# Kernel optimization log

Measured on AMD Instinct MI355X. Metric: run time of the kernel, lower is better.

## Reference

```python
import jax, jax.numpy as jnp
import numpy as np

MAXV = 8  # convex quad clipped by 4 half-planes has <= 8 vertices


def decode(enc, anchors):
    """ResidualCoder.decode_torch for 7-dof lidar boxes (x,y,z,dx,dy,dz,r)."""
    xa, ya, za, dxa, dya, dza, ra = [anchors[..., i] for i in range(7)]
    xt, yt, zt, dxt, dyt, dzt, rt = [enc[..., i] for i in range(7)]
    diag = jnp.sqrt(dxa * dxa + dya * dya)
    xg = xt * diag + xa
    yg = yt * diag + ya
    zg = zt * dza + za
    dxg = jnp.exp(dxt) * dxa
    dyg = jnp.exp(dyt) * dya
    dzg = jnp.exp(dzt) * dza
    rg = rt + ra
    return jnp.stack([xg, yg, zg, dxg, dyg, dzg, rg], axis=-1)


def bev_corners(boxes):
    # boxes (...,7) -> CCW BEV corners (...,4,2) using x,y,dx,dy,heading
    x, y, dx, dy, r = boxes[..., 0], boxes[..., 1], boxes[..., 3], boxes[..., 4], boxes[..., 6]
    cx = jnp.stack([dx, -dx, -dx, dx], -1) * 0.5
    cy = jnp.stack([dy, dy, -dy, -dy], -1) * 0.5
    c, s = jnp.cos(r)[..., None], jnp.sin(r)[..., None]
    px = cx * c - cy * s + x[..., None]
    py = cx * s + cy * c + y[..., None]
    return jnp.stack([px, py], -1)


def _clip(poly, n, A, B):
    """Sutherland-Hodgman clip of polygon (poly[:n]) by half-plane left of A->B."""
    idx = jnp.arange(MAXV)
    e = B - A
    s = e[0] * (poly[:, 1] - A[1]) - e[1] * (poly[:, 0] - A[0])  # signed side
    prev = (idx - 1) % jnp.maximum(n, 1)
    s_prev = s[prev]
    p_prev = poly[prev]
    active = idx < n
    cin = s >= 0
    pin = s_prev >= 0
    den = s_prev - s
    t = s_prev / jnp.where(den == 0, 1.0, den)
    inter = p_prev + t[:, None] * (poly - p_prev)
    f_int = active & (cin != pin)   # edge crosses boundary -> emit intersection
    f_cur = active & cin            # current vertex inside -> emit it
    cand = jnp.stack([inter, poly], 1).reshape(2 * MAXV, 2)
    flags = jnp.stack([f_int, f_cur], 1).reshape(2 * MAXV)
    pos = jnp.cumsum(flags) - 1
    new_n = pos[-1] + 1
    pos = jnp.where(flags, pos, MAXV)  # invalid -> dump slot
    out = jnp.zeros((MAXV + 1, 2), poly.dtype).at[pos].set(cand)[:MAXV]
    return out, new_n.astype(jnp.int32)


def _pair_iou_bev(c1, c2, a1, a2):
    # c1,c2: (4,2) CCW corners of the two rotated BEV boxes; a1,a2: scalar areas
    poly = jnp.zeros((MAXV, 2), c1.dtype).at[:4].set(c1)
    n = jnp.asarray(4, jnp.int32)
    for e in range(4):
        poly, n = _clip(poly, n, c2[e], c2[(e + 1) % 4])
    idx = jnp.arange(MAXV)
    nxt = (idx + 1) % jnp.maximum(n, 1)
    x, y = poly[:, 0], poly[:, 1]
    contrib = jnp.where(idx < n, x * y[nxt] - x[nxt] * y, 0.0)
    inter = 0.5 * jnp.abs(contrib.sum())
    return inter / jnp.clip(a1 + a2 - inter, 1e-6, None)


def rotated_iou_bev_diag(boxes1, boxes2):
    """Diagonal (elementwise) rotated BEV IoU for flattened (M,7) lidar boxes."""
    c1 = bev_corners(boxes1)
    c2 = bev_corners(boxes2)
    a1 = boxes1[..., 3] * boxes1[..., 4]
    a2 = boxes2[..., 3] * boxes2[..., 4]
    return jax.vmap(_pair_iou_bev)(c1, c2, a1, a2)


def setup_inputs() -> dict:
    key = jax.random.key(0)
    ks = jax.random.split(key, 8)
    B, N = 4, 262144
    iou_preds = jax.random.normal(ks[0], (B, N), jnp.float32)
    one_hot_targets = jax.random.randint(ks[1], (B, N), 0, 2, jnp.int32)
    weights = jax.random.uniform(ks[2], (B, N), jnp.float32)
    # realistic anchors: xy in [-50,50], z ~ -1, dims in [1.5,4.5], heading in [0,pi)
    xy = jax.random.uniform(ks[3], (N, 2), jnp.float32, -50.0, 50.0)
    z = jnp.full((N, 1), -1.0, jnp.float32)
    dims = jax.random.uniform(ks[4], (N, 3), jnp.float32, 1.5, 4.5)
    ang = jax.random.uniform(ks[5], (N, 1), jnp.float32, 0.0, np.pi)
    anchors = jnp.concatenate([xy, z, dims, ang], axis=-1)
    box_preds = 0.1 * jax.random.normal(ks[6], (B, N, 7), jnp.float32)
    reg_targets = 0.1 * jax.random.normal(ks[7], (B, N, 7), jnp.float32)
    return {"iou_preds": iou_preds, "one_hot_targets": one_hot_targets,
            "weights": weights, "anchors": anchors,
            "box_preds": box_preds, "reg_targets": reg_targets}


def reference(iou_preds, one_hot_targets, weights, anchors, box_preds, reg_targets):
    B, N = iou_preds.shape
    dec_pred = decode(box_preds, anchors[None, :, :])   # (B,N,7)
    dec_tgt = decode(reg_targets, anchors[None, :, :])  # (B,N,7)
    iou = rotated_iou_bev_diag(dec_pred.reshape(B * N, 7),
                               dec_tgt.reshape(B * N, 7)).reshape(B, N)
    # label is computed with no grad, only at positive anchors; zero elsewhere
    target = jax.lax.stop_gradient(jnp.where(one_hot_targets > 0, iou, 0.0))
    # faithful to the original quirk: BCE-with-logits applied to sigmoid(iou_preds)
    z = jax.nn.sigmoid(iou_preds)
    p_t = jnp.logaddexp(0.0, z) - z * target  # log(1+e^z) - t*z
    return p_t * weights
```

## Files before the change

kernel.cpp:

```cpp
#include <hip/hip_runtime.h>
#include <math.h>

#define BLK 256
#define MAXV 8


__device__ __forceinline__ void clip_first(float* __restrict__ PX, float* __restrict__ PY,
                                           int tid,
                                           const float qx[4], const float qy[4],
                                           int& n, float& lastx, float& lasty,
                                           float Ax, float Ay, float Bx, float By)
{
    float ex = Bx - Ax, ey = By - Ay;
    float s0 = ex * (qy[0] - Ay) - ey * (qx[0] - Ax);
    float s1 = ex * (qy[1] - Ay) - ey * (qx[1] - Ax);
    float s2 = ex * (qy[2] - Ay) - ey * (qx[2] - Ax);
    float s3 = ex * (qy[3] - Ay) - ey * (qx[3] - Ax);
    float vs[4] = {s0, s1, s2, s3};

    float ppx = qx[3], ppy = qy[3], ps = s3;
    int m = 0;
    float lx = ppx, ly = ppy;
#pragma unroll
    for (int i = 0; i < 4; ++i) {
        float cx = qx[i], cy = qy[i], cs = vs[i];
        bool cin = (cs >= 0.0f), pin = (ps >= 0.0f);
        if (cin != pin) {
            float den = ps - cs;
            den = (den == 0.0f) ? 1.0f : den;
            float t = __fdividef(ps, den);
            float ix = fmaf(t, cx - ppx, ppx);
            float iy = fmaf(t, cy - ppy, ppy);
            if (m < MAXV) { PX[m * BLK + tid] = ix; PY[m * BLK + tid] = iy; }
            lx = ix; ly = iy; ++m;
        }
        if (cin) {
            if (m < MAXV) { PX[m * BLK + tid] = cx; PY[m * BLK + tid] = cy; }
            lx = cx; ly = cy; ++m;
        }
        ppx = cx; ppy = cy; ps = cs;
    }
    n = (m < MAXV) ? m : MAXV;
    lastx = lx; lasty = ly;
}

template<int NIN>
__device__ __forceinline__ void clip_mid(float* __restrict__ PX, float* __restrict__ PY,
                                         int tid, int& n, float& lastx, float& lasty,
                                         float Ax, float Ay, float Bx, float By)
{
    float ex = Bx - Ax, ey = By - Ay;
    float vx[NIN], vy[NIN], vs[NIN];
#pragma unroll
    for (int i = 0; i < NIN; ++i) {
        vx[i] = PX[i * BLK + tid];
        vy[i] = PY[i * BLK + tid];
        vs[i] = ex * (vy[i] - Ay) - ey * (vx[i] - Ax);
    }
    float ppx = lastx, ppy = lasty;
    float ps = ex * (ppy - Ay) - ey * (ppx - Ax);
    int m = 0;
    float lx = lastx, ly = lasty;
#pragma unroll
    for (int i = 0; i < NIN; ++i) {
        if (i < n) {
            float cx = vx[i], cy = vy[i], cs = vs[i];
            bool cin = (cs >= 0.0f), pin = (ps >= 0.0f);
            if (cin != pin) {
                float den = ps - cs;
                den = (den == 0.0f) ? 1.0f : den;
                float t = __fdividef(ps, den);
                float ix = fmaf(t, cx - ppx, ppx);
                float iy = fmaf(t, cy - ppy, ppy);
                if (m < MAXV) { PX[m * BLK + tid] = ix; PY[m * BLK + tid] = iy; }
                lx = ix; ly = iy; ++m;
            }
            if (cin) {
                if (m < MAXV) { PX[m * BLK + tid] = cx; PY[m * BLK + tid] = cy; }
                lx = cx; ly = cy; ++m;
            }
            ppx = cx; ppy = cy; ps = cs;
        }
    }
    n = (m < MAXV) ? m : MAXV;
    lastx = lx; lasty = ly;
}

template<int NIN>
__device__ __forceinline__ float clip_area(const float* __restrict__ PX,
                                           const float* __restrict__ PY,
                                           int tid, int n, float lastx, float lasty,
                                           float Ax, float Ay, float Bx, float By)
{
    float ex = Bx - Ax, ey = By - Ay;
    float ppx = lastx, ppy = lasty;
    float ps = ex * (ppy - Ay) - ey * (ppx - Ax);
    int m = 0;
    float fx = 0.0f, fy = 0.0f, lx = 0.0f, ly = 0.0f, area2 = 0.0f;
#pragma unroll
    for (int i = 0; i < NIN; ++i) {
        if (i < n) {
            float cx = PX[i * BLK + tid], cy = PY[i * BLK + tid];
            float cs = ex * (cy - Ay) - ey * (cx - Ax);
            bool cin = (cs >= 0.0f), pin = (ps >= 0.0f);
            if (cin != pin) {
                float den = ps - cs;
                den = (den == 0.0f) ? 1.0f : den;
                float t = __fdividef(ps, den);
                float ix = fmaf(t, cx - ppx, ppx);
                float iy = fmaf(t, cy - ppy, ppy);
                if (m == 0) { fx = ix; fy = iy; }
                else        { area2 += lx * iy - ix * ly; }
                lx = ix; ly = iy; ++m;
            }
            if (cin) {
                if (m == 0) { fx = cx; fy = cy; }
                else        { area2 += lx * cy - cx * ly; }
                lx = cx; ly = cy; ++m;
            }
            ppx = cx; ppy = cy; ps = cs;
        }
    }
    if (m > 0) area2 += lx * fy - fx * ly;
    return 0.5f * fabsf(area2);
}

__global__ __launch_bounds__(BLK)
void iou_pred_loss_kernel(const float* __restrict__ iou_preds,
                          const int*   __restrict__ one_hot,
                          const float* __restrict__ weights,
                          const float* __restrict__ anchors,
                          const float* __restrict__ box_preds,
                          const float* __restrict__ reg_targets,
                          float* __restrict__ out,
                          int N, int total)
{
    __shared__ float sPX[MAXV][BLK];
    __shared__ float sPY[MAXV][BLK];

    int tid = threadIdx.x;
    int gid = blockIdx.x * BLK + tid;
    if (gid >= total) return;

    int n_idx = gid % N;

    const float* an = anchors + (size_t)n_idx * 7;
    float xa = an[0], ya = an[1], dxa = an[3], dya = an[4], ra = an[6];
    float diag = sqrtf(dxa * dxa + dya * dya);

    const float* bp = box_preds + (size_t)gid * 7;
    float x1  = fmaf(bp[0], diag, xa);
    float y1  = fmaf(bp[1], diag, ya);
    float dx1 = __expf(bp[3]) * dxa;
    float dy1 = __expf(bp[4]) * dya;
    float r1  = bp[6] + ra;

    const float* rt = reg_targets + (size_t)gid * 7;
    float x2  = fmaf(rt[0], diag, xa);
    float y2  = fmaf(rt[1], diag, ya);
    float dx2 = __expf(rt[3]) * dxa;
    float dy2 = __expf(rt[4]) * dya;
    float r2  = rt[6] + ra;

    float a1 = dx1 * dy1;
    float a2 = dx2 * dy2;

    float c1 = __cosf(r1), s1 = __sinf(r1);
    float hx1 = 0.5f * dx1, hy1 = 0.5f * dy1;
    float q1x[4], q1y[4];
    q1x[0] =  hx1 * c1 - hy1 * s1 + x1;  q1y[0] =  hx1 * s1 + hy1 * c1 + y1;
    q1x[1] = -hx1 * c1 - hy1 * s1 + x1;  q1y[1] = -hx1 * s1 + hy1 * c1 + y1;
    q1x[2] = -hx1 * c1 + hy1 * s1 + x1;  q1y[2] = -hx1 * s1 - hy1 * c1 + y1;
    q1x[3] =  hx1 * c1 + hy1 * s1 + x1;  q1y[3] =  hx1 * s1 - hy1 * c1 + y1;

    float c2 = __cosf(r2), s2 = __sinf(r2);
    float hx2 = 0.5f * dx2, hy2 = 0.5f * dy2;
    float q2x[4], q2y[4];
    q2x[0] =  hx2 * c2 - hy2 * s2 + x2;  q2y[0] =  hx2 * s2 + hy2 * c2 + y2;
    q2x[1] = -hx2 * c2 - hy2 * s2 + x2;  q2y[1] = -hx2 * s2 + hy2 * c2 + y2;
    q2x[2] = -hx2 * c2 + hy2 * s2 + x2;  q2y[2] = -hx2 * s2 - hy2 * c2 + y2;
    q2x[3] =  hx2 * c2 + hy2 * s2 + x2;  q2y[3] =  hx2 * s2 - hy2 * c2 + y2;

    float* PX = &sPX[0][0];
    float* PY = &sPY[0][0];
    int   n;
    float lastx, lasty;
    clip_first(PX, PY, tid, q1x, q1y, n, lastx, lasty,
               q2x[0], q2y[0], q2x[1], q2y[1]);
    clip_mid<6>(PX, PY, tid, n, lastx, lasty,
                q2x[1], q2y[1], q2x[2], q2y[2]);
    clip_mid<7>(PX, PY, tid, n, lastx, lasty,
                q2x[2], q2y[2], q2x[3], q2y[3]);
    float inter = clip_area<8>(PX, PY, tid, n, lastx, lasty,
                               q2x[3], q2y[3], q2x[0], q2y[0]);

    float uni = a1 + a2 - inter;
    uni = fmaxf(uni, 1e-6f);
    float iou = __fdividef(inter, uni);

    float target = (one_hot[gid] > 0) ? iou : 0.0f;
    float ip = iou_preds[gid];
    float z  = __fdividef(1.0f, 1.0f + __expf(-ip));
    float pt = __logf(1.0f + __expf(z)) - z * target;
    out[gid] = pt * weights[gid];
}

extern "C" void kernel_launch(void* const* d_in, const int* in_sizes, int n_in,
                              void* d_out, int out_size, void* d_ws, size_t ws_size,
                              hipStream_t stream) {
    const float* iou_preds   = (const float*)d_in[0];
    const int*   one_hot     = (const int*)  d_in[1];
    const float* weights     = (const float*)d_in[2];
    const float* anchors     = (const float*)d_in[3];
    const float* box_preds   = (const float*)d_in[4];
    const float* reg_targets = (const float*)d_in[5];
    float* out = (float*)d_out;

    int total = in_sizes[0];
    int N     = in_sizes[3] / 7;

    int blocks = (total + BLK - 1) / BLK;
    iou_pred_loss_kernel<<<blocks, BLK, 0, stream>>>(
        iou_preds, one_hot, weights, anchors, box_preds, reg_targets,
        out, N, total);
}
```

Before: 123.7 us.

## Clip in box-2 local frame with axis-aligned half-planes and branchless writes

Transforms box 1 into box 2's local coordinate frame, so the four clipping half-planes become axis-aligned tests (K - y, x + K, etc.) rather than general edge cross-products. The clip loops become branchless by writing to a spare shared-memory slot when a vertex is not emitted, and polygon vertices are stored as float2. The grid becomes 2D (anchor by batch), which removes the integer modulo. This cuts arithmetic and wavefront divergence, at the cost of always doing the divisions and stores and of small rounding differences from the changed frame.

```diff
diff --git a/kernel.cpp b/kernel.cpp
--- a/kernel.cpp
+++ b/kernel.cpp
@@ -2,126 +2,121 @@
 #include <math.h>
 
 #define BLK 256
-#define MAXV 8
-
-
-__device__ __forceinline__ void clip_first(float* __restrict__ PX, float* __restrict__ PY,
-                                           int tid,
-                                           const float qx[4], const float qy[4],
-                                           int& n, float& lastx, float& lasty,
-                                           float Ax, float Ay, float Bx, float By)
-{
-    float ex = Bx - Ax, ey = By - Ay;
-    float s0 = ex * (qy[0] - Ay) - ey * (qx[0] - Ax);
-    float s1 = ex * (qy[1] - Ay) - ey * (qx[1] - Ax);
-    float s2 = ex * (qy[2] - Ay) - ey * (qx[2] - Ax);
-    float s3 = ex * (qy[3] - Ay) - ey * (qx[3] - Ax);
-    float vs[4] = {s0, s1, s2, s3};
-
-    float ppx = qx[3], ppy = qy[3], ps = s3;
-    int m = 0;
-    float lx = ppx, ly = ppy;
+#define SPARE 8
+
+
+template<int MODE>
+__device__ __forceinline__ float sfun(float x, float y, float K) {
+    if (MODE == 0) return K - y;
+    if (MODE == 1) return x + K;
+    if (MODE == 2) return y + K;
+    return K - x;
+}
+
+template<int MODE>
+__device__ __forceinline__ int clip_first(float2* __restrict__ P, int tid,
+                                          const float qx[4], const float qy[4],
+                                          float K)
+{
+    float ppx = qx[3], ppy = qy[3];
+    float ps  = sfun<MODE>(ppx, ppy, K);
+    bool  pin = ps >= 0.0f;
+    int   m   = 0;
 #pragma unroll
     for (int i = 0; i < 4; ++i) {
-        float cx = qx[i], cy = qy[i], cs = vs[i];
-        bool cin = (cs >= 0.0f), pin = (ps >= 0.0f);
-        if (cin != pin) {
-            float den = ps - cs;
-            den = (den == 0.0f) ? 1.0f : den;
-            float t = __fdividef(ps, den);
-            float ix = fmaf(t, cx - ppx, ppx);
-            float iy = fmaf(t, cy - ppy, ppy);
-            if (m < MAXV) { PX[m * BLK + tid] = ix; PY[m * BLK + tid] = iy; }
-            lx = ix; ly = iy; ++m;
-        }
-        if (cin) {
-            if (m < MAXV) { PX[m * BLK + tid] = cx; PY[m * BLK + tid] = cy; }
-            lx = cx; ly = cy; ++m;
-        }
-        ppx = cx; ppy = cy; ps = cs;
-    }
-    n = (m < MAXV) ? m : MAXV;
-    lastx = lx; lasty = ly;
-}
-
-template<int NIN>
-__device__ __forceinline__ void clip_mid(float* __restrict__ PX, float* __restrict__ PY,
-                                         int tid, int& n, float& lastx, float& lasty,
-                                         float Ax, float Ay, float Bx, float By)
-{
-    float ex = Bx - Ax, ey = By - Ay;
+        float cx = qx[i], cy = qy[i];
+        float cs = sfun<MODE>(cx, cy, K);
+        bool  cin = cs >= 0.0f;
+        bool  fi  = (cin != pin);
+        float t  = __fdividef(ps, ps - cs);
+        float ix = fmaf(t, cx - ppx, ppx);
+        float iy = fmaf(t, cy - ppy, ppy);
+        int si = fi ? m : SPARE;
+        P[si * BLK + tid] = make_float2(ix, iy);
+        m += fi;
+        int sc = cin ? m : SPARE;
+        P[sc * BLK + tid] = make_float2(cx, cy);
+        m += cin;
+        ppx = cx; ppy = cy; ps = cs; pin = cin;
+    }
+    return m;
+}
+
+template<int MODE, int NIN>
+__device__ __forceinline__ int clip_mid(float2* __restrict__ P, int tid,
+                                        int n, float K)
+{
     float vx[NIN], vy[NIN], vs[NIN];
 #pragma unroll
     for (int i = 0; i < NIN; ++i) {
-        vx[i] = PX[i * BLK + tid];
-        vy[i] = PY[i * BLK + tid];
-        vs[i] = ex * (vy[i] - Ay) - ey * (vx[i] - Ax);
-    }
-    float ppx = lastx, ppy = lasty;
-    float ps = ex * (ppy - Ay) - ey * (ppx - Ax);
-    int m = 0;
-    float lx = lastx, ly = lasty;
+        float2 v = P[i * BLK + tid];
+        vx[i] = v.x; vy[i] = v.y;
+        vs[i] = sfun<MODE>(v.x, v.y, K);
+    }
+    int pslot = n - 1; pslot = pslot < 0 ? 0 : pslot;
+    float2 pv = P[pslot * BLK + tid];
+    float ppx = pv.x, ppy = pv.y;
+    float ps  = sfun<MODE>(ppx, ppy, K);
+    bool  pin = ps >= 0.0f;
+    int   m   = 0;
 #pragma unroll
     for (int i = 0; i < NIN; ++i) {
-        if (i < n) {
-            float cx = vx[i], cy = vy[i], cs = vs[i];
-            bool cin = (cs >= 0.0f), pin = (ps >= 0.0f);
-            if (cin != pin) {
-                float den = ps - cs;
-                den = (den == 0.0f) ? 1.0f : den;
-                float t = __fdividef(ps, den);
-                float ix = fmaf(t, cx - ppx, ppx);
-                float iy = fmaf(t, cy - ppy, ppy);
-                if (m < MAXV) { PX[m * BLK + tid] = ix; PY[m * BLK + tid] = iy; }
-                lx = ix; ly = iy; ++m;
-            }
-            if (cin) {
-                if (m < MAXV) { PX[m * BLK + tid] = cx; PY[m * BLK + tid] = cy; }
-                lx = cx; ly = cy; ++m;
-            }
-            ppx = cx; ppy = cy; ps = cs;
-        }
-    }
-    n = (m < MAXV) ? m : MAXV;
-    lastx = lx; lasty = ly;
-}
-
-template<int NIN>
-__device__ __forceinline__ float clip_area(const float* __restrict__ PX,
-                                           const float* __restrict__ PY,
-                                           int tid, int n, float lastx, float lasty,
-                                           float Ax, float Ay, float Bx, float By)
-{
-    float ex = Bx - Ax, ey = By - Ay;
-    float ppx = lastx, ppy = lasty;
-    float ps = ex * (ppy - Ay) - ey * (ppx - Ax);
-    int m = 0;
+        bool  act = i < n;
+        float cx = vx[i], cy = vy[i], cs = vs[i];
+        bool  cin = cs >= 0.0f;
+        bool  fi  = act && (cin != pin);
+        bool  fc  = act && cin;
+        float t  = __fdividef(ps, ps - cs);
+        float ix = fmaf(t, cx - ppx, ppx);
+        float iy = fmaf(t, cy - ppy, ppy);
+        int si = fi ? m : SPARE;
+        P[si * BLK + tid] = make_float2(ix, iy);
+        m += fi;
+        int sc = fc ? m : SPARE;
+        P[sc * BLK + tid] = make_float2(cx, cy);
+        m += fc;
+        ppx = cx; ppy = cy; ps = cs; pin = cin;
+    }
+    return m;
+}
+
+template<int MODE, int NIN>
+__device__ __forceinline__ float clip_area(const float2* __restrict__ P, int tid,
+                                           int n, float K)
+{
+    int pslot = n - 1; pslot = pslot < 0 ? 0 : pslot;
+    float2 pv = P[pslot * BLK + tid];
+    float ppx = pv.x, ppy = pv.y;
+    float ps  = sfun<MODE>(ppx, ppy, K);
+    bool  pin = ps >= 0.0f;
+    bool  seen = false;
     float fx = 0.0f, fy = 0.0f, lx = 0.0f, ly = 0.0f, area2 = 0.0f;
 #pragma unroll
     for (int i = 0; i < NIN; ++i) {
-        if (i < n) {
-            float cx = PX[i * BLK + tid], cy = PY[i * BLK + tid];
-            float cs = ex * (cy - Ay) - ey * (cx - Ax);
-            bool cin = (cs >= 0.0f), pin = (ps >= 0.0f);
-            if (cin != pin) {
-                float den = ps - cs;
-                den = (den == 0.0f) ? 1.0f : den;
-                float t = __fdividef(ps, den);
-                float ix = fmaf(t, cx - ppx, ppx);
-                float iy = fmaf(t, cy - ppy, ppy);
-                if (m == 0) { fx = ix; fy = iy; }
-                else        { area2 += lx * iy - ix * ly; }
-                lx = ix; ly = iy; ++m;
-            }
-            if (cin) {
-                if (m == 0) { fx = cx; fy = cy; }
-                else        { area2 += lx * cy - cx * ly; }
-                lx = cx; ly = cy; ++m;
-            }
-            ppx = cx; ppy = cy; ps = cs;
-        }
-    }
-    if (m > 0) area2 += lx * fy - fx * ly;
+        float2 v = P[i * BLK + tid];
+        float cx = v.x, cy = v.y;
+        float cs = sfun<MODE>(cx, cy, K);
+        bool  act = i < n;
+        bool  cin = cs >= 0.0f;
+        bool  fi  = act && (cin != pin);
+        bool  fc  = act && cin;
+        float t  = __fdividef(ps, ps - cs);
+        float ix = fmaf(t, cx - ppx, ppx);
+        float iy = fmaf(t, cy - ppy, ppy);
+        float c1 = fmaf(lx, iy, -(ix * ly));
+        area2 += (fi && seen) ? c1 : 0.0f;
+        fx = (fi && !seen) ? ix : fx;  fy = (fi && !seen) ? iy : fy;
+        lx = fi ? ix : lx;             ly = fi ? iy : ly;
+        seen = seen || fi;
+        float c2 = fmaf(lx, cy, -(cx * ly));
+        area2 += (fc && seen) ? c2 : 0.0f;
+        fx = (fc && !seen) ? cx : fx;  fy = (fc && !seen) ? cy : fy;
+        lx = fc ? cx : lx;             ly = fc ? cy : ly;
+        seen = seen || fc;
+        ppx = cx; ppy = cy; ps = cs; pin = cin;
+    }
+    float wrap = fmaf(lx, fy, -(fx * ly));
+    area2 += seen ? wrap : 0.0f;
     return 0.5f * fabsf(area2);
 }
 
@@ -133,20 +128,18 @@
                           const float* __restrict__ box_preds,
                           const float* __restrict__ reg_targets,
                           float* __restrict__ out,
-                          int N, int total)
-{
-    __shared__ float sPX[MAXV][BLK];
-    __shared__ float sPY[MAXV][BLK];
-
-    int tid = threadIdx.x;
-    int gid = blockIdx.x * BLK + tid;
-    if (gid >= total) return;
-
-    int n_idx = gid % N;
+                          int N)
+{
+    __shared__ float2 sP[(SPARE + 1) * BLK];
+
+    int tid   = threadIdx.x;
+    int n_idx = blockIdx.x * BLK + tid;
+    if (n_idx >= N) return;
+    int gid = blockIdx.y * N + n_idx;
 
     const float* an = anchors + (size_t)n_idx * 7;
     float xa = an[0], ya = an[1], dxa = an[3], dya = an[4], ra = an[6];
-    float diag = sqrtf(dxa * dxa + dya * dya);
+    float diag = sqrtf(fmaf(dxa, dxa, dya * dya));
 
     const float* bp = box_preds + (size_t)gid * 7;
     float x1  = fmaf(bp[0], diag, xa);
@@ -165,34 +158,29 @@
     float a1 = dx1 * dy1;
     float a2 = dx2 * dy2;
 
-    float c1 = __cosf(r1), s1 = __sinf(r1);
-    float hx1 = 0.5f * dx1, hy1 = 0.5f * dy1;
-    float q1x[4], q1y[4];
-    q1x[0] =  hx1 * c1 - hy1 * s1 + x1;  q1y[0] =  hx1 * s1 + hy1 * c1 + y1;
-    q1x[1] = -hx1 * c1 - hy1 * s1 + x1;  q1y[1] = -hx1 * s1 + hy1 * c1 + y1;
-    q1x[2] = -hx1 * c1 + hy1 * s1 + x1;  q1y[2] = -hx1 * s1 - hy1 * c1 + y1;
-    q1x[3] =  hx1 * c1 + hy1 * s1 + x1;  q1y[3] =  hx1 * s1 - hy1 * c1 + y1;
-
-    float c2 = __cosf(r2), s2 = __sinf(r2);
-    float hx2 = 0.5f * dx2, hy2 = 0.5f * dy2;
-    float q2x[4], q2y[4];
-    q2x[0] =  hx2 * c2 - hy2 * s2 + x2;  q2y[0] =  hx2 * s2 + hy2 * c2 + y2;
-    q2x[1] = -hx2 * c2 - hy2 * s2 + x2;  q2y[1] = -hx2 * s2 + hy2 * c2 + y2;
-    q2x[2] = -hx2 * c2 + hy2 * s2 + x2;  q2y[2] = -hx2 * s2 - hy2 * c2 + y2;
-    q2x[3] =  hx2 * c2 + hy2 * s2 + x2;  q2y[3] =  hx2 * s2 - hy2 * c2 + y2;
-
-    float* PX = &sPX[0][0];
-    float* PY = &sPY[0][0];
-    int   n;
-    float lastx, lasty;
-    clip_first(PX, PY, tid, q1x, q1y, n, lastx, lasty,
-               q2x[0], q2y[0], q2x[1], q2y[1]);
-    clip_mid<6>(PX, PY, tid, n, lastx, lasty,
-                q2x[1], q2y[1], q2x[2], q2y[2]);
-    clip_mid<7>(PX, PY, tid, n, lastx, lasty,
-                q2x[2], q2y[2], q2x[3], q2y[3]);
-    float inter = clip_area<8>(PX, PY, tid, n, lastx, lasty,
-                               q2x[3], q2y[3], q2x[0], q2y[0]);
+    float c2v = __cosf(r2), s2v = __sinf(r2);
+    float dr  = r1 - r2;
+    float cd  = __cosf(dr), sd = __sinf(dr);
+    float ddx = x1 - x2, ddy = y1 - y2;
+    float tx  = fmaf(c2v, ddx,  s2v * ddy);
+    float ty  = fmaf(-s2v, ddx, c2v * ddy);
+    float h1x = 0.5f * dx1, h1y = 0.5f * dy1;
+    float h2x = 0.5f * dx2, h2y = 0.5f * dy2;
+    float e1x = h1x * cd,  e1y = h1x * sd;
+    float e2x = -h1y * sd, e2y = h1y * cd;
+    float qx[4], qy[4];
+    qx[0] = tx + e1x + e2x;  qy[0] = ty + e1y + e2y;
+    qx[1] = tx - e1x + e2x;  qy[1] = ty - e1y + e2y;
+    qx[2] = tx - e1x - e2x;  qy[2] = ty - e1y - e2y;
+    qx[3] = tx + e1x - e2x;  qy[3] = ty + e1y - e2y;
+
+    int m = clip_first<0>(sP, tid, qx, qy, h2y);
+    int n = m < 6 ? m : 6;
+    m = clip_mid<1, 6>(sP, tid, n, h2x);
+    n = m < 7 ? m : 7;
+    m = clip_mid<2, 7>(sP, tid, n, h2y);
+    n = m < 8 ? m : 8;
+    float inter = clip_area<3, 8>(sP, tid, n, h2x);
 
     float uni = a1 + a2 - inter;
     uni = fmaxf(uni, 1e-6f);
@@ -218,9 +206,10 @@
 
     int total = in_sizes[0];
     int N     = in_sizes[3] / 7;
-
-    int blocks = (total + BLK - 1) / BLK;
-    iou_pred_loss_kernel<<<blocks, BLK, 0, stream>>>(
+    int B     = total / N;
+
+    dim3 grid((N + BLK - 1) / BLK, B);
+    iou_pred_loss_kernel<<<grid, dim3(BLK), 0, stream>>>(
         iou_preds, one_hot, weights, anchors, box_preds, reg_targets,
-        out, N, total);
-}
+        out, N);
+}
```

After: 121.6 us. About the same (-1.8%).
